# Optimization experiments

Measured on AMD Instinct MI355X. Metric: run time of the kernel, lower is better.

## Reference

```python
import jax, jax.numpy as jnp
import numpy as np

N_AE = 512
N_DE = 256
N = 100000
NUM_SEG = 1024
EPS = 1e-5


def setup_inputs() -> dict:
    key = jax.random.key(0)
    ks = jax.random.split(key, 20)
    d_in1 = 2 * N_AE + N_DE  # 1280
    inp = {
        "x": jax.random.normal(ks[0], (N, 2 * N_AE), dtype=jnp.float32),
        "dist_feat": jax.random.normal(ks[1], (N, N_DE), dtype=jnp.float32),
        "atom_idx": jax.random.randint(ks[2], (N,), 0, 100, dtype=jnp.int32),
        "ele_idx": jax.random.randint(ks[3], (N,), 0, NUM_SEG, dtype=jnp.int32),
        # layer 1 params
        "l1_w": jax.random.normal(ks[4], (d_in1, N_AE), dtype=jnp.float32) * (1.0 / np.sqrt(d_in1)),
        "l1_b": jnp.zeros((N_AE,), dtype=jnp.float32),
        "l1_g": jnp.ones((N_AE,), dtype=jnp.float32),
        "l1_be": jnp.zeros((N_AE,), dtype=jnp.float32),
        # layer 2 params (same input width: 2*n_ae + n_de)
        "l2_w": jax.random.normal(ks[5], (d_in1, N_AE), dtype=jnp.float32) * (1.0 / np.sqrt(d_in1)),
        "l2_b": jnp.zeros((N_AE,), dtype=jnp.float32),
        "l2_g": jnp.ones((N_AE,), dtype=jnp.float32),
        "l2_be": jnp.zeros((N_AE,), dtype=jnp.float32),
        # final fc + bn
        "f_w": jax.random.normal(ks[6], (2 * N_AE, N_AE), dtype=jnp.float32) * (1.0 / np.sqrt(2 * N_AE)),
        "f_b": jnp.zeros((N_AE,), dtype=jnp.float32),
        "f_g": jnp.ones((N_AE,), dtype=jnp.float32),
        "f_be": jnp.zeros((N_AE,), dtype=jnp.float32),
    }
    return inp


def _bn(h, gamma, beta):
    # BatchNorm1d in training mode: batch stats, biased variance
    m = jnp.mean(h, axis=0)
    v = jnp.mean(jnp.square(h - m), axis=0)
    return gamma * (h - m) * jax.lax.rsqrt(v + EPS) + beta


def _dist_layer(x_cat, ele_idx, w, b, gamma, beta):
    h = jax.nn.relu(_bn(x_cat @ w + b, gamma, beta))  # [N, n_ae]
    sums = jax.ops.segment_sum(h, ele_idx, num_segments=NUM_SEG)  # [S, n_ae]
    cnt = jax.ops.segment_sum(jnp.ones((h.shape[0],), h.dtype), ele_idx, num_segments=NUM_SEG)
    mean = sums / jnp.maximum(cnt, 1.0)[:, None]
    return jnp.concatenate([h, mean[ele_idx]], axis=1)  # [N, 2*n_ae]


def reference(x, dist_feat, atom_idx, ele_idx,
              l1_w, l1_b, l1_g, l1_be,
              l2_w, l2_b, l2_g, l2_be,
              f_w, f_b, f_g, f_be):
    h = _dist_layer(jnp.concatenate([x, dist_feat], axis=1), ele_idx, l1_w, l1_b, l1_g, l1_be)
    h = _dist_layer(jnp.concatenate([h, dist_feat], axis=1), ele_idx, l2_w, l2_b, l2_g, l2_be)
    out = jax.nn.relu(_bn(h @ f_w + f_b, f_g, f_be))  # [N, n_ae]
    return out
```

## Files before the change

### kernel.cpp

```cpp
#include <hip/hip_runtime.h>
#include <stdint.h>
#include <stdio.h>

#define NOUT 512
#define NSEG 1024

typedef unsigned short u16;
typedef __attribute__((ext_vector_type(4))) float f32x4;
typedef __attribute__((ext_vector_type(8))) short s16x8;
typedef __attribute__((ext_vector_type(4))) unsigned short u16x4;

__device__ __forceinline__ u16 f2b(float f) {
  union { float f; uint32_t u; } v; v.f = f;
  uint32_t r = v.u + 0x7FFFu + ((v.u >> 16) & 1u);
  return (u16)(r >> 16);
}
__device__ __forceinline__ float b2f(u16 b) {
  union { uint32_t u; float f; } v; v.u = ((uint32_t)b) << 16;
  return v.f;
}

typedef __attribute__((address_space(1))) const void GAS;
typedef __attribute__((address_space(3))) void LAS;
__device__ __forceinline__ void llds16(const void* g, void* l) {
  __builtin_amdgcn_global_load_lds((GAS*)g, (LAS*)l, 16, 0, 0);
}

__global__ void k_cast(const float* __restrict__ src, u16* __restrict__ dst, long n4) {
  long i = blockIdx.x * (long)blockDim.x + threadIdx.x;
  long stride = (long)gridDim.x * blockDim.x;
  for (; i < n4; i += stride) {
    float4 v = reinterpret_cast<const float4*>(src)[i];
    u16x4 o;
    o.x = f2b(v.x); o.y = f2b(v.y); o.z = f2b(v.z); o.w = f2b(v.w);
    reinterpret_cast<u16x4*>(dst)[i] = o;
  }
}

__global__ void k_wtcastT(const float* __restrict__ w, u16* __restrict__ out, int K) {
  __shared__ float tile[32][33];
  int k0 = blockIdx.x * 32, c0 = blockIdx.y * 32;
  int t = threadIdx.x;
  int rr = t >> 5, cc = t & 31;
#pragma unroll
  for (int p = 0; p < 4; ++p)
    tile[p * 8 + rr][cc] = w[(long)(k0 + p * 8 + rr) * NOUT + c0 + cc];
  __syncthreads();
#pragma unroll
  for (int p = 0; p < 4; ++p)
    out[(long)(c0 + p * 8 + rr) * K + k0 + cc] = f2b(tile[cc][p * 8 + rr]);
}

__global__ void k_hist(const int* __restrict__ ele, int* __restrict__ cnt, int N) {
  int i = blockIdx.x * blockDim.x + threadIdx.x;
  int stride = gridDim.x * blockDim.x;
  for (; i < N; i += stride) atomicAdd(&cnt[ele[i]], 1);
}

__global__ void k_scan(const int* __restrict__ cnt, int* __restrict__ off) {
  __shared__ int tmp[NSEG];
  int t = threadIdx.x;
  tmp[t] = cnt[t];
  __syncthreads();
  for (int o = 1; o < NSEG; o <<= 1) {
    int add = (t >= o) ? tmp[t - o] : 0;
    __syncthreads();
    tmp[t] += add;
    __syncthreads();
  }
  off[t] = tmp[t] - cnt[t];
}

__global__ void k_scatter(const int* __restrict__ ele, const int* __restrict__ off,
                          int* __restrict__ fill, int* __restrict__ rows, int N) {
  int i = blockIdx.x * blockDim.x + threadIdx.x;
  int stride = gridDim.x * blockDim.x;
  for (; i < N; i += stride) {
    int e = ele[i];
    int p = atomicAdd(&fill[e], 1);
    rows[off[e] + p] = i;
  }
}

__global__ void k_finalize(const float* __restrict__ sum, const float* __restrict__ sumsq,
                           const float* __restrict__ g, const float* __restrict__ be,
                           float* __restrict__ A, float* __restrict__ C, int M) {
  int c = threadIdx.x;
  float m = sum[c] / (float)M;
  float v = sumsq[c] / (float)M - m * m;
  float a = g[c] * rsqrtf(v + 1e-5f);
  A[c] = a;
  C[c] = be[c] - a * m;
}

__global__ void k_bnseg(const u16* __restrict__ hp, u16* __restrict__ h, u16* __restrict__ mean,
                        const float* __restrict__ A, const float* __restrict__ C,
                        const int* __restrict__ off, const int* __restrict__ cnt,
                        const int* __restrict__ rows) {
  int s = blockIdx.x;
  int c0 = blockIdx.y * 256 + 2 * threadIdx.x;
  int n = cnt[s], o = off[s];
  float a0 = A[c0], a1 = A[c0 + 1], cc0 = C[c0], cc1 = C[c0 + 1];
  float s0 = 0.f, s1 = 0.f;
  for (int j = 0; j < n; ++j) {
    int r = rows[o + j];
    uint32_t v = *reinterpret_cast<const uint32_t*>(&hp[(long)r * NOUT + c0]);
    float h0 = fmaxf(a0 * b2f((u16)(v & 0xffff)) + cc0, 0.f);
    float h1 = fmaxf(a1 * b2f((u16)(v >> 16)) + cc1, 0.f);
    s0 += h0; s1 += h1;
    *reinterpret_cast<uint32_t*>(&h[(long)r * NOUT + c0]) =
        ((uint32_t)f2b(h1) << 16) | (uint32_t)f2b(h0);
  }
  float inv = 1.f / fmaxf((float)n, 1.f);
  *reinterpret_cast<uint32_t*>(&mean[(long)s * NOUT + c0]) =
      ((uint32_t)f2b(s1 * inv) << 16) | (uint32_t)f2b(s0 * inv);
}

__global__ void k_final(const u16* __restrict__ hp, float* __restrict__ out,
                        const float* __restrict__ A, const float* __restrict__ C, long n4) {
  long i = blockIdx.x * (long)blockDim.x + threadIdx.x;
  long stride = (long)gridDim.x * blockDim.x;
  for (; i < n4; i += stride) {
    u16x4 v = reinterpret_cast<const u16x4*>(hp)[i];
    int c0 = (int)((i * 4) & (NOUT - 1));
    float4 a = *reinterpret_cast<const float4*>(&A[c0]);
    float4 c = *reinterpret_cast<const float4*>(&C[c0]);
    float4 o;
    o.x = fmaxf(a.x * b2f(v.x) + c.x, 0.f);
    o.y = fmaxf(a.y * b2f(v.y) + c.y, 0.f);
    o.z = fmaxf(a.z * b2f(v.z) + c.z, 0.f);
    o.w = fmaxf(a.w * b2f(v.w) + c.w, 0.f);
    reinterpret_cast<float4*>(out)[i] = o;
  }
}

__global__ __launch_bounds__(256, 2) void k_gemm(
    const u16* p0, const u16* p1, int e0, int w0, int w1, int g0, int g1,
    const int* __restrict__ ele,
    const u16* __restrict__ wbt, int ldb, int e0b, int bskip,
    const float* __restrict__ tab, int addtab,
    u16* __restrict__ outp, float* __restrict__ outf, int wf32,
    float* __restrict__ csum, float* __restrict__ csq, int dostats,
    int M, int K) {
  __shared__ __align__(16) u16 As[128 * 64];
  __shared__ __align__(16) u16 Bs[256 * 64];

  int nwg = gridDim.x;
  int orig = blockIdx.x;
  int q = nwg >> 3, r8 = nwg & 7;
  int xcd = orig & 7, loc = orig >> 3;
  int bid = (xcd < r8 ? xcd * (q + 1) : r8 * (q + 1) + (xcd - r8) * q) + loc;
  int mt = bid >> 1, ct = bid & 1;
  int brow = mt * 128, bcol = ct * 256;

  int tid = (int)threadIdx.x;
  int lane = tid & 63;
  int wid = tid >> 6;
  int wr = wid >> 1, wc = wid & 1;
  int l15 = lane & 15, kg = lane >> 4;

  int rl = tid >> 3;
  int soct = ((tid & 7) ^ (rl & 7)) * 8;

  int rida0[4], rida1[4];
#pragma unroll
  for (int c = 0; c < 4; ++c) {
    int gr = brow + rl + 32 * c;
    if (gr >= M) gr = M - 1;
    int e = (g0 | g1) ? ele[gr] : 0;
    rida0[c] = g0 ? e : gr;
    rida1[c] = g1 ? e : gr;
  }
  const u16* bptr[8];
#pragma unroll
  for (int c = 0; c < 8; ++c)
    bptr[c] = wbt + (long)(bcol + rl + 32 * c) * ldb + soct;

  int ch0 = (kg ^ (l15 & 7)) * 8;
  int ch1 = ((4 | kg) ^ (l15 & 7)) * 8;
  int arow = (wr * 64 + l15) * 64;
  int brow_l = (wc * 128 + l15) * 64;

  f32x4 acc[4][8];
#pragma unroll
  for (int m = 0; m < 4; ++m)
#pragma unroll
    for (int n = 0; n < 8; ++n)
#pragma unroll
      for (int j = 0; j < 4; ++j) acc[m][n][j] = 0.f;

  int KT = K >> 6;
  for (int t = 0; t < KT; ++t) {
    int k0 = t << 6;
    __syncthreads();
    if (k0 < e0) {
#pragma unroll
      for (int c = 0; c < 4; ++c)
        llds16(p0 + (long)rida0[c] * w0 + soct + k0, &As[c * 2048 + wid * 512]);
    } else {
      int ko = k0 - e0;
#pragma unroll
      for (int c = 0; c < 4; ++c)
        llds16(p1 + (long)rida1[c] * w1 + soct + ko, &As[c * 2048 + wid * 512]);
    }
    int bo = k0 + (k0 >= e0b ? bskip : 0);
#pragma unroll
    for (int c = 0; c < 8; ++c)
      llds16(bptr[c] + bo, &Bs[c * 2048 + wid * 512]);
    __syncthreads();
#pragma unroll
    for (int kk = 0; kk < 2; ++kk) {
      int ch = kk ? ch1 : ch0;
      s16x8 af[4], bf[8];
#pragma unroll
      for (int m = 0; m < 4; ++m)
        af[m] = *reinterpret_cast<const s16x8*>(&As[arow + m * 1024 + ch]);
#pragma unroll
      for (int n = 0; n < 8; ++n)
        bf[n] = *reinterpret_cast<const s16x8*>(&Bs[brow_l + n * 1024 + ch]);
#pragma unroll
      for (int m = 0; m < 4; ++m)
#pragma unroll
        for (int n = 0; n < 8; ++n)
          acc[m][n] = __builtin_amdgcn_mfma_f32_16x16x32_bf16(af[m], bf[n], acc[m][n], 0, 0, 0);
    }
  }

  float sums[8], sqs[8];
#pragma unroll
  for (int n = 0; n < 8; ++n) { sums[n] = 0.f; sqs[n] = 0.f; }
#pragma unroll
  for (int m = 0; m < 4; ++m) {
    int row0 = brow + wr * 64 + m * 16 + kg * 4;
#pragma unroll
    for (int j = 0; j < 4; ++j) {
      int r = row0 + j;
      if (r < M) {
        long rb = (long)r * NOUT;
        long tb = addtab ? (long)ele[r] * NOUT : 0;
#pragma unroll
        for (int n = 0; n < 8; ++n) {
          int col = bcol + wc * 128 + n * 16 + l15;
          float v = acc[m][n][j];
          if (addtab) v += tab[tb + col];
          if (wf32) outf[rb + col] = v;
          else outp[rb + col] = f2b(v);
          sums[n] += v;
          sqs[n] += v * v;
        }
      }
    }
  }
  if (dostats) {
#pragma unroll
    for (int n = 0; n < 8; ++n) {
      sums[n] += __shfl_xor(sums[n], 16);
      sums[n] += __shfl_xor(sums[n], 32);
      sqs[n] += __shfl_xor(sqs[n], 16);
      sqs[n] += __shfl_xor(sqs[n], 32);
    }
    if (kg == 0) {
#pragma unroll
      for (int n = 0; n < 8; ++n) {
        int col = bcol + wc * 128 + n * 16 + l15;
        atomicAdd(&csum[col], sums[n]);
        atomicAdd(&csq[col], sqs[n]);
      }
    }
  }
}

extern "C" void kernel_launch(void* const* d_in, const int* in_sizes, int n_in,
                              void* d_out, int out_size, void* d_ws, size_t ws_size,
                              hipStream_t stream) {
  const float* x    = (const float*)d_in[0];
  const float* dist = (const float*)d_in[1];
  const int* ele    = (const int*)d_in[3];
  const float* l1w  = (const float*)d_in[4];
  const float* l1g  = (const float*)d_in[6];
  const float* l1be = (const float*)d_in[7];
  const float* l2w  = (const float*)d_in[8];
  const float* l2g  = (const float*)d_in[10];
  const float* l2be = (const float*)d_in[11];
  const float* fw   = (const float*)d_in[12];
  const float* fg   = (const float*)d_in[14];
  const float* fbe  = (const float*)d_in[15];

  int N = in_sizes[0] / 1024;
  float* out = (float*)d_out;
  u16* xbf = (u16*)d_out;

  int MT = (N + 127) / 128;

  char* w = (char*)d_ws;
  auto alloc = [&](size_t bytes) {
    char* p = w;
    w += (bytes + 255) & ~(size_t)255;
    return p;
  };
  u16* dist_bf = (u16*)alloc((size_t)N * 256 * 2);
  u16* hp      = (u16*)alloc((size_t)N * NOUT * 2);
  u16* h       = (u16*)alloc((size_t)N * NOUT * 2);
  u16* mean    = (u16*)alloc((size_t)NSEG * NOUT * 2);
  u16* w1bt    = (u16*)alloc((size_t)NOUT * 1280 * 2);
  u16* w2bt    = (u16*)alloc((size_t)NOUT * 1280 * 2);
  u16* fbt     = (u16*)alloc((size_t)NOUT * 1024 * 2);
  float* mc2   = (float*)alloc((size_t)NSEG * NOUT * 4);
  float* mc3   = (float*)alloc((size_t)NSEG * NOUT * 4);
  float* colsum = (float*)alloc(NOUT * 4 * 2);
  float* colsumsq = colsum + NOUT;
  float* bnA   = (float*)alloc(NOUT * 4);
  float* bnC   = (float*)alloc(NOUT * 4);
  int* seg_cnt = (int*)alloc(NSEG * 4);
  int* seg_off = (int*)alloc(NSEG * 4);
  int* seg_fill = (int*)alloc(NSEG * 4);
  int* rows    = (int*)alloc((size_t)N * 4);

  size_t need = (size_t)(w - (char*)d_ws);
  if (need > ws_size) {
    fprintf(stderr, "kernel_launch: ws too small: need %zu have %zu\n", need, ws_size);
    return;
  }

  long n4x = (long)N * 1024 / 4;
  long n4d = (long)N * 256 / 4;
  long n4h = (long)N * NOUT / 4;
  int gemmGrid = MT * 2;
  int mcGrid = (NSEG / 128) * 2;
  dim3 bnsegGrid(NSEG, 2);

  k_cast<<<4096, 256, 0, stream>>>(x, xbf, n4x);
  k_cast<<<2048, 256, 0, stream>>>(dist, dist_bf, n4d);
  dim3 wt1(1280 / 32, 16), wt3(1024 / 32, 16);
  k_wtcastT<<<wt1, 256, 0, stream>>>(l1w, w1bt, 1280);
  k_wtcastT<<<wt1, 256, 0, stream>>>(l2w, w2bt, 1280);
  k_wtcastT<<<wt3, 256, 0, stream>>>(fw, fbt, 1024);

  hipMemsetAsync(seg_cnt, 0, NSEG * 4, stream);
  hipMemsetAsync(seg_fill, 0, NSEG * 4, stream);
  k_hist<<<512, 256, 0, stream>>>(ele, seg_cnt, N);
  k_scan<<<1, NSEG, 0, stream>>>(seg_cnt, seg_off);
  k_scatter<<<512, 256, 0, stream>>>(ele, seg_off, seg_fill, rows, N);

  hipMemsetAsync(colsum, 0, NOUT * 4 * 2, stream);
  k_gemm<<<gemmGrid, 256, 0, stream>>>(xbf, dist_bf, 1024, 1024, 256, 0, 0, ele,
                                       w1bt, 1280, 1280, 0, mc2, 0,
                                       hp, mc2, 0, colsum, colsumsq, 1, N, 1280);
  k_finalize<<<1, NOUT, 0, stream>>>(colsum, colsumsq, l1g, l1be, bnA, bnC, N);
  k_bnseg<<<bnsegGrid, 128, 0, stream>>>(hp, h, mean, bnA, bnC, seg_off, seg_cnt, rows);

  k_gemm<<<mcGrid, 256, 0, stream>>>(mean, mean, 512, 512, 512, 0, 0, ele,
                                     w2bt + 512, 1280, 512, 0, mc2, 0,
                                     hp, mc2, 1, colsum, colsumsq, 0, NSEG, 512);
  hipMemsetAsync(colsum, 0, NOUT * 4 * 2, stream);
  k_gemm<<<gemmGrid, 256, 0, stream>>>(h, dist_bf, 512, 512, 256, 0, 0, ele,
                                       w2bt, 1280, 512, 512, mc2, 1,
                                       hp, mc2, 0, colsum, colsumsq, 1, N, 768);
  k_finalize<<<1, NOUT, 0, stream>>>(colsum, colsumsq, l2g, l2be, bnA, bnC, N);
  k_bnseg<<<bnsegGrid, 128, 0, stream>>>(hp, h, mean, bnA, bnC, seg_off, seg_cnt, rows);

  k_gemm<<<mcGrid, 256, 0, stream>>>(mean, mean, 512, 512, 512, 0, 0, ele,
                                     fbt + 512, 1024, 512, 0, mc3, 0,
                                     hp, mc3, 1, colsum, colsumsq, 0, NSEG, 512);
  hipMemsetAsync(colsum, 0, NOUT * 4 * 2, stream);
  k_gemm<<<gemmGrid, 256, 0, stream>>>(h, h, 512, 512, 512, 0, 0, ele,
                                       fbt, 1024, 512, 0, mc3, 1,
                                       hp, mc3, 0, colsum, colsumsq, 1, N, 512);
  k_finalize<<<1, NOUT, 0, stream>>>(colsum, colsumsq, fg, fbe, bnA, bnC, N);
  k_final<<<4096, 256, 0, stream>>>(hp, out, bnA, bnC, n4h);
}
```

Measured before the change: 1.107 ms.

## Double-buffer GEMM LDS tiles with 128x128 tiles and K-step 32

```diff
diff --git a/kernel.cpp b/kernel.cpp
--- a/kernel.cpp
+++ b/kernel.cpp
@@ -98,7 +98,7 @@
                         const int* __restrict__ off, const int* __restrict__ cnt,
                         const int* __restrict__ rows) {
   int s = blockIdx.x;
-  int c0 = blockIdx.y * 256 + 2 * threadIdx.x;
+  int c0 = blockIdx.y * 128 + 2 * threadIdx.x;
   int n = cnt[s], o = off[s];
   float a0 = A[c0], a1 = A[c0 + 1], cc0 = C[c0], cc1 = C[c0 + 1];
   float s0 = 0.f, s1 = 0.f;
@@ -134,7 +134,7 @@
   }
 }
 
-__global__ __launch_bounds__(256, 2) void k_gemm(
+__global__ __launch_bounds__(256, 3) void k_gemm(
     const u16* p0, const u16* p1, int e0, int w0, int w1, int g0, int g1,
     const int* __restrict__ ele,
     const u16* __restrict__ wbt, int ldb, int e0b, int bskip,
@@ -142,16 +142,16 @@
     u16* __restrict__ outp, float* __restrict__ outf, int wf32,
     float* __restrict__ csum, float* __restrict__ csq, int dostats,
     int M, int K) {
-  __shared__ __align__(16) u16 As[128 * 64];
-  __shared__ __align__(16) u16 Bs[256 * 64];
+  __shared__ __align__(16) u16 As[2 * 4096];
+  __shared__ __align__(16) u16 Bs[2 * 4096];
 
   int nwg = gridDim.x;
   int orig = blockIdx.x;
   int q = nwg >> 3, r8 = nwg & 7;
   int xcd = orig & 7, loc = orig >> 3;
   int bid = (xcd < r8 ? xcd * (q + 1) : r8 * (q + 1) + (xcd - r8) * q) + loc;
-  int mt = bid >> 1, ct = bid & 1;
-  int brow = mt * 128, bcol = ct * 256;
+  int mt = bid >> 2, ct = bid & 3;
+  int brow = mt * 128, bcol = ct * 128;
 
   int tid = (int)threadIdx.x;
   int lane = tid & 63;
@@ -159,76 +159,74 @@
   int wr = wid >> 1, wc = wid & 1;
   int l15 = lane & 15, kg = lane >> 4;
 
-  int rl = tid >> 3;
-  int soct = ((tid & 7) ^ (rl & 7)) * 8;
-
-  int rida0[4], rida1[4];
-#pragma unroll
-  for (int c = 0; c < 4; ++c) {
-    int gr = brow + rl + 32 * c;
-    if (gr >= M) gr = M - 1;
-    int e = (g0 | g1) ? ele[gr] : 0;
-    rida0[c] = g0 ? e : gr;
-    rida1[c] = g1 ? e : gr;
-  }
-  const u16* bptr[8];
-#pragma unroll
-  for (int c = 0; c < 8; ++c)
-    bptr[c] = wbt + (long)(bcol + rl + 32 * c) * ldb + soct;
-
-  int ch0 = (kg ^ (l15 & 7)) * 8;
-  int ch1 = ((4 | kg) ^ (l15 & 7)) * 8;
-  int arow = (wr * 64 + l15) * 64;
-  int brow_l = (wc * 128 + l15) * 64;
-
-  f32x4 acc[4][8];
+  int srow = tid >> 2;
+  int soct = ((tid & 3) ^ ((srow >> 1) & 3)) * 8;
+
+  int gr0 = brow + srow, gr1 = gr0 + 64;
+  int gr0c = gr0 < M ? gr0 : M - 1;
+  int gr1c = gr1 < M ? gr1 : M - 1;
+  int el0 = ele[gr0c], el1 = ele[gr1c];
+
+  const u16* a00 = p0 + (long)(g0 ? el0 : gr0c) * w0 + soct;
+  const u16* a01 = p1 + (long)(g1 ? el0 : gr0c) * w1 + soct - e0;
+  const u16* a10 = p0 + (long)(g0 ? el1 : gr1c) * w0 + soct;
+  const u16* a11 = p1 + (long)(g1 ? el1 : gr1c) * w1 + soct - e0;
+
+  const u16* b0p = wbt + (long)(bcol + srow) * ldb + soct;
+  const u16* b1p = wbt + (long)(bcol + srow + 64) * ldb + soct;
+
+  int xoct = (kg ^ ((l15 >> 1) & 3)) * 8;
+  int aro = (wr * 64 + l15) * 32 + xoct;
+  int bro = (wc * 64 + l15) * 32 + xoct;
+
+  f32x4 acc[4][4];
 #pragma unroll
   for (int m = 0; m < 4; ++m)
 #pragma unroll
-    for (int n = 0; n < 8; ++n)
+    for (int n = 0; n < 4; ++n)
 #pragma unroll
       for (int j = 0; j < 4; ++j) acc[m][n][j] = 0.f;
 
-  int KT = K >> 6;
+  int KT = K >> 5;
+  int dst = wid * 512;
+
+  auto stage = [&](int tt, int buf) {
+    int k0 = tt << 5;
+    const u16* sa0 = k0 < e0 ? a00 : a01;
+    const u16* sa1 = k0 < e0 ? a10 : a11;
+    int bo = k0 + (k0 >= e0b ? bskip : 0);
+    int ab = buf * 4096 + dst;
+    llds16(sa0 + k0, &As[ab]);
+    llds16(sa1 + k0, &As[ab + 2048]);
+    llds16(b0p + bo, &Bs[ab]);
+    llds16(b1p + bo, &Bs[ab + 2048]);
+  };
+
+  stage(0, 0);
+  __syncthreads();
+
   for (int t = 0; t < KT; ++t) {
-    int k0 = t << 6;
+    int cur = t & 1;
+    if (t + 1 < KT) stage(t + 1, cur ^ 1);
+    __builtin_amdgcn_sched_barrier(0);
+    const u16* Ab = &As[cur * 4096];
+    const u16* Bb = &Bs[cur * 4096];
+    s16x8 af[4], bf[4];
+#pragma unroll
+    for (int m = 0; m < 4; ++m)
+      af[m] = *reinterpret_cast<const s16x8*>(&Ab[m * 512 + aro]);
+#pragma unroll
+    for (int n = 0; n < 4; ++n)
+      bf[n] = *reinterpret_cast<const s16x8*>(&Bb[n * 512 + bro]);
+#pragma unroll
+    for (int m = 0; m < 4; ++m)
+#pragma unroll
+      for (int n = 0; n < 4; ++n)
+        acc[m][n] = __builtin_amdgcn_mfma_f32_16x16x32_bf16(af[m], bf[n], acc[m][n], 0, 0, 0);
     __syncthreads();
-    if (k0 < e0) {
-#pragma unroll
-      for (int c = 0; c < 4; ++c)
-        llds16(p0 + (long)rida0[c] * w0 + soct + k0, &As[c * 2048 + wid * 512]);
-    } else {
-      int ko = k0 - e0;
-#pragma unroll
-      for (int c = 0; c < 4; ++c)
-        llds16(p1 + (long)rida1[c] * w1 + soct + ko, &As[c * 2048 + wid * 512]);
-    }
-    int bo = k0 + (k0 >= e0b ? bskip : 0);
-#pragma unroll
-    for (int c = 0; c < 8; ++c)
-      llds16(bptr[c] + bo, &Bs[c * 2048 + wid * 512]);
-    __syncthreads();
-#pragma unroll
-    for (int kk = 0; kk < 2; ++kk) {
-      int ch = kk ? ch1 : ch0;
-      s16x8 af[4], bf[8];
-#pragma unroll
-      for (int m = 0; m < 4; ++m)
-        af[m] = *reinterpret_cast<const s16x8*>(&As[arow + m * 1024 + ch]);
-#pragma unroll
-      for (int n = 0; n < 8; ++n)
-        bf[n] = *reinterpret_cast<const s16x8*>(&Bs[brow_l + n * 1024 + ch]);
-#pragma unroll
-      for (int m = 0; m < 4; ++m)
-#pragma unroll
-        for (int n = 0; n < 8; ++n)
-          acc[m][n] = __builtin_amdgcn_mfma_f32_16x16x32_bf16(af[m], bf[n], acc[m][n], 0, 0, 0);
-    }
-  }
-
-  float sums[8], sqs[8];
-#pragma unroll
-  for (int n = 0; n < 8; ++n) { sums[n] = 0.f; sqs[n] = 0.f; }
+  }
+
+  float sums[4] = {0.f, 0.f, 0.f, 0.f}, sqs[4] = {0.f, 0.f, 0.f, 0.f};
 #pragma unroll
   for (int m = 0; m < 4; ++m) {
     int row0 = brow + wr * 64 + m * 16 + kg * 4;
@@ -239,8 +237,8 @@
         long rb = (long)r * NOUT;
         long tb = addtab ? (long)ele[r] * NOUT : 0;
 #pragma unroll
-        for (int n = 0; n < 8; ++n) {
-          int col = bcol + wc * 128 + n * 16 + l15;
+        for (int n = 0; n < 4; ++n) {
+          int col = bcol + wc * 64 + n * 16 + l15;
           float v = acc[m][n][j];
           if (addtab) v += tab[tb + col];
           if (wf32) outf[rb + col] = v;
@@ -253,7 +251,7 @@
   }
   if (dostats) {
 #pragma unroll
-    for (int n = 0; n < 8; ++n) {
+    for (int n = 0; n < 4; ++n) {
       sums[n] += __shfl_xor(sums[n], 16);
       sums[n] += __shfl_xor(sums[n], 32);
       sqs[n] += __shfl_xor(sqs[n], 16);
@@ -261,8 +259,8 @@
     }
     if (kg == 0) {
 #pragma unroll
-      for (int n = 0; n < 8; ++n) {
-        int col = bcol + wc * 128 + n * 16 + l15;
+      for (int n = 0; n < 4; ++n) {
+        int col = bcol + wc * 64 + n * 16 + l15;
         atomicAdd(&csum[col], sums[n]);
         atomicAdd(&csq[col], sqs[n]);
       }
@@ -325,9 +323,9 @@
   long n4x = (long)N * 1024 / 4;
   long n4d = (long)N * 256 / 4;
   long n4h = (long)N * NOUT / 4;
-  int gemmGrid = MT * 2;
-  int mcGrid = (NSEG / 128) * 2;
-  dim3 bnsegGrid(NSEG, 2);
+  int gemmGrid = MT * 4;
+  int mcGrid = (NSEG / 128) * 4;
+  dim3 bnsegGrid(NSEG, 4);
 
   k_cast<<<4096, 256, 0, stream>>>(x, xbf, n4x);
   k_cast<<<2048, 256, 0, stream>>>(dist, dist_bf, n4d);
@@ -347,7 +345,7 @@
                                        w1bt, 1280, 1280, 0, mc2, 0,
                                        hp, mc2, 0, colsum, colsumsq, 1, N, 1280);
   k_finalize<<<1, NOUT, 0, stream>>>(colsum, colsumsq, l1g, l1be, bnA, bnC, N);
-  k_bnseg<<<bnsegGrid, 128, 0, stream>>>(hp, h, mean, bnA, bnC, seg_off, seg_cnt, rows);
+  k_bnseg<<<bnsegGrid, 64, 0, stream>>>(hp, h, mean, bnA, bnC, seg_off, seg_cnt, rows);
 
   k_gemm<<<mcGrid, 256, 0, stream>>>(mean, mean, 512, 512, 512, 0, 0, ele,
                                      w2bt + 512, 1280, 512, 0, mc2, 0,
@@ -357,7 +355,7 @@
                                        w2bt, 1280, 512, 512, mc2, 1,
                                        hp, mc2, 0, colsum, colsumsq, 1, N, 768);
   k_finalize<<<1, NOUT, 0, stream>>>(colsum, colsumsq, l2g, l2be, bnA, bnC, N);
-  k_bnseg<<<bnsegGrid, 128, 0, stream>>>(hp, h, mean, bnA, bnC, seg_off, seg_cnt, rows);
+  k_bnseg<<<bnsegGrid, 64, 0, stream>>>(hp, h, mean, bnA, bnC, seg_off, seg_cnt, rows);
 
   k_gemm<<<mcGrid, 256, 0, stream>>>(mean, mean, 512, 512, 512, 0, 0, ele,
                                      fbt + 512, 1024, 512, 0, mc3, 0,
```

After: 988.3 us. 10.8% less time.
